# Performance work log

Hardware: AMD Instinct MI355X
Metric: run time of the kernel (lower is better)

The kernel has to match this reference:

```python
import jax, jax.numpy as jnp
import numpy as np

B, N, D_MODEL, H = 2, 2048, 1024, 16
HD = D_MODEL // H  # head_dim = 64

def setup_inputs() -> dict:
    key = jax.random.key(0)
    ks = jax.random.split(key, 5)
    x = jax.random.normal(ks[0], (B, N, D_MODEL), dtype=jnp.float32)
    scale = 0.02
    # Linear weights stored as [in, out] (torch does x @ W.T with W [out,in]; equivalent math)
    Wq = jax.random.normal(ks[1], (D_MODEL, D_MODEL), dtype=jnp.float32) * scale
    Wk = jax.random.normal(ks[2], (D_MODEL, D_MODEL), dtype=jnp.float32) * scale
    Wv = jax.random.normal(ks[3], (D_MODEL, D_MODEL), dtype=jnp.float32) * scale
    Wo = jax.random.normal(ks[4], (D_MODEL, D_MODEL), dtype=jnp.float32) * scale
    return {"x": x, "Wq": Wq, "Wk": Wk, "Wv": Wv, "Wo": Wo}

def reference(x, Wq, Wk, Wv, Wo):
    b, n, _ = x.shape
    # QKV projections (no bias; qkv_bias=False)
    q = (x @ Wq).reshape(b, n, H, HD)
    k = (x @ Wk).reshape(b, n, H, HD)
    v = (x @ Wv).reshape(b, n, H, HD)
    # scores [b, h, q, k]
    scores = jnp.einsum('bqhd,bkhd->bhqk', q, k) / jnp.sqrt(jnp.float32(HD))
    causal = jnp.triu(jnp.ones((n, n), dtype=bool), k=1)  # True above diagonal -> masked
    scores = jnp.where(causal, -jnp.inf, scores)
    attn = jax.nn.softmax(scores, axis=-1)  # dropout p=0.0 -> identity
    ctx = jnp.einsum('bhqk,bkhd->bqhd', attn, v).reshape(b, n, D_MODEL)
    return ctx @ Wo
```

## Files before the change

kernel.cpp:

```cpp
#include <hip/hip_runtime.h>
#include <math.h>

#define D_MODEL 1024
#define NHEAD 16
#define HD 64
#define SEQ 2048
#define BATCH 2
#define MTOT (BATCH * SEQ)

typedef __attribute__((ext_vector_type(8))) short bf16x8;
typedef __attribute__((ext_vector_type(4))) float f32x4;

__device__ __forceinline__ unsigned short f2bf(float f) {
    unsigned int u = __float_as_uint(f);
    u += 0x7FFF + ((u >> 16) & 1);
    return (unsigned short)(u >> 16);
}

__device__ __forceinline__ unsigned int pk2bf(float a, float b) {
    unsigned int r;
    asm("v_cvt_pk_bf16_f32 %0, %1, %2" : "=v"(r) : "v"(a), "v"(b));
    return r;
}

__device__ __forceinline__ void async16(unsigned short* lds, const unsigned short* g) {
    __builtin_amdgcn_global_load_lds(
        (const __attribute__((address_space(1))) unsigned int*)g,
        (__attribute__((address_space(3))) unsigned int*)lds, 16, 0, 0);
}

__global__ __launch_bounds__(256) void prep(const float* __restrict__ x,
                                            unsigned short* __restrict__ xb,
                                            const float* __restrict__ W0,
                                            const float* __restrict__ W1,
                                            const float* __restrict__ W2,
                                            const float* __restrict__ W3,
                                            unsigned short* __restrict__ Wt) {
    const int bid = blockIdx.x;
    const int tid = threadIdx.x;
    if (bid < 4096) {
        const int i = (bid * 256 + tid) * 4;
        float4 v = *(const float4*)(x + i);
        uint2 pk;
        pk.x = pk2bf(v.x, v.y);
        pk.y = pk2bf(v.z, v.w);
        *(uint2*)(xb + i) = pk;
    } else {
        __shared__ float T[32][33];
        const int t = bid - 4096;
        const int z = t >> 10, rem = t & 1023;
        const int n0 = (rem & 31) * 32, k0 = (rem >> 5) * 32;
        const float* W = (z == 0) ? W0 : (z == 1) ? W1 : (z == 2) ? W2 : W3;
        unsigned short* out = Wt + (size_t)z * D_MODEL * D_MODEL;
        const int tx = tid & 31, ty = tid >> 5;
#pragma unroll
        for (int i = 0; i < 4; ++i)
            T[ty + 8 * i][tx] = W[(size_t)(k0 + ty + 8 * i) * D_MODEL + n0 + tx];
        __syncthreads();
#pragma unroll
        for (int i = 0; i < 4; ++i)
            out[(size_t)(n0 + ty + 8 * i) * D_MODEL + k0 + tx] = f2bf(T[tx][ty + 8 * i]);
    }
}

template <int MODE>
__global__ __launch_bounds__(256) void gemm_mfma(const unsigned short* __restrict__ A,
                                                 const unsigned short* __restrict__ Wt,
                                                 unsigned short* __restrict__ q,
                                                 unsigned short* __restrict__ k,
                                                 unsigned short* __restrict__ vt,
                                                 float* __restrict__ outf) {
    __shared__ unsigned short SM[16384];
    const int tid = threadIdx.x;
    const int z = blockIdx.z;
    const unsigned short* B = Wt + (size_t)z * D_MODEL * D_MODEL;
    const int m0 = blockIdx.y * 128, n0 = blockIdx.x * 128;
    const int wave = tid >> 6, lane = tid & 63;
    const int quad = lane >> 4, l16 = lane & 15;
    const int wm = wave & 1, wn = wave >> 1;

    f32x4 acc[4][4];
#pragma unroll
    for (int mt = 0; mt < 4; ++mt)
#pragma unroll
        for (int nt = 0; nt < 4; ++nt)
            acc[mt][nt] = (f32x4){0.f, 0.f, 0.f, 0.f};

    for (int k0 = 0; k0 < D_MODEL; k0 += 64) {
        __syncthreads();
#pragma unroll
        for (int i = 0; i < 4; ++i) {
            const int c = i * 256 + tid;
            const int r = c >> 3, cc = (c & 7) * 8;
            const int cbase = i * 256 + wave * 64;
            async16(SM + cbase * 8, A + (size_t)(m0 + r) * D_MODEL + k0 + cc);
            async16(SM + 8192 + cbase * 8, B + (size_t)(n0 + r) * D_MODEL + k0 + cc);
        }
        __syncthreads();
#pragma unroll
        for (int ks = 0; ks < 2; ++ks) {
            bf16x8 af[4], bfr[4];
#pragma unroll
            for (int mt = 0; mt < 4; ++mt)
                af[mt] = *(const bf16x8*)&SM[(wm * 64 + mt * 16 + l16) * 64 + ks * 32 + quad * 8];
#pragma unroll
            for (int nt = 0; nt < 4; ++nt)
                bfr[nt] = *(const bf16x8*)&SM[8192 + (wn * 64 + nt * 16 + l16) * 64 + ks * 32 + quad * 8];
#pragma unroll
            for (int mt = 0; mt < 4; ++mt)
#pragma unroll
                for (int nt = 0; nt < 4; ++nt)
                    acc[mt][nt] = __builtin_amdgcn_mfma_f32_16x16x32_bf16(
                        af[mt], bfr[nt], acc[mt][nt], 0, 0, 0);
        }
    }

    if (MODE == 1) {
#pragma unroll
        for (int mt = 0; mt < 4; ++mt)
#pragma unroll
            for (int nt = 0; nt < 4; ++nt)
#pragma unroll
                for (int reg = 0; reg < 4; ++reg) {
                    const int m = m0 + wm * 64 + mt * 16 + quad * 4 + reg;
                    const int n = n0 + wn * 64 + nt * 16 + l16;
                    outf[(size_t)m * D_MODEL + n] = acc[mt][nt][reg];
                }
    } else if (z < 2) {
        const float qsc = (z == 0) ? 0.18033688011112042f : 1.0f;
        unsigned short* dst = (z == 0) ? q : k;
        const int bb = m0 >> 11;
        const int tok0 = m0 & (SEQ - 1);
        const int h0 = n0 >> 6;
#pragma unroll
        for (int pass = 0; pass < 2; ++pass) {
            __syncthreads();
            if (wm == pass) {
#pragma unroll
                for (int mt = 0; mt < 4; ++mt)
#pragma unroll
                    for (int nt = 0; nt < 4; ++nt)
#pragma unroll
                        for (int reg = 0; reg < 4; ++reg) {
                            const int r = mt * 16 + quad * 4 + reg;
                            const int cc = wn * 64 + nt * 16 + l16;
                            SM[r * 128 + cc] = f2bf(acc[mt][nt][reg] * qsc);
                        }
            }
            __syncthreads();
#pragma unroll
            for (int it = 0; it < 4; ++it) {
                const int cix = it * 256 + tid;
                const int r = cix >> 4, g = cix & 15;
                const int hh = g >> 3, d8 = g & 7;
                uint4 val = *(const uint4*)&SM[r * 128 + g * 8];
                *(uint4*)(dst + (((size_t)bb * NHEAD + h0 + hh) * SEQ +
                                 tok0 + pass * 64 + r) * HD + d8 * 8) = val;
            }
        }
    } else {
        const int bb = m0 >> 11, tok0 = m0 & (SEQ - 1);
#pragma unroll
        for (int pass = 0; pass < 2; ++pass) {
            __syncthreads();
            if (wn == pass) {
#pragma unroll
                for (int mt = 0; mt < 4; ++mt)
#pragma unroll
                    for (int nt = 0; nt < 4; ++nt) {
                        const int d = nt * 16 + l16;
                        const int m = wm * 64 + mt * 16 + quad * 4;
                        uint2 w;
                        w.x = pk2bf(acc[mt][nt][0], acc[mt][nt][1]);
                        w.y = pk2bf(acc[mt][nt][2], acc[mt][nt][3]);
                        *(uint2*)&SM[d * 136 + m] = w;
                    }
            }
            __syncthreads();
            const int h = (n0 >> 6) + pass;
#pragma unroll
            for (int it = 0; it < 4; ++it) {
                const int c = it * 256 + tid;
                const int d = c >> 4, mc = (c & 15) * 8;
                uint4 val = *(const uint4*)&SM[d * 136 + mc];
                *(uint4*)(vt + (((size_t)bb * NHEAD + h) * HD + d) * SEQ + tok0 + mc) = val;
            }
        }
    }
}

__global__ __launch_bounds__(256, 2) void attn_mfma(const unsigned short* __restrict__ Q,
                                                    const unsigned short* __restrict__ K,
                                                    const unsigned short* __restrict__ VT,
                                                    unsigned short* __restrict__ ctx) {
    __shared__ float CMB[8832];
    const int tid = threadIdx.x;
    const int wave = tid >> 6, lane = tid & 63;
    const int quad = lane >> 4, l16 = lane & 15;
    const int h = blockIdx.x, b = blockIdx.z;
    const int y = blockIdx.y;
    const unsigned short* Qp = Q + ((size_t)b * NHEAD + h) * SEQ * HD;
    const unsigned short* Kp = K + ((size_t)b * NHEAD + h) * SEQ * HD;
    const unsigned short* Vp = VT + ((size_t)b * NHEAD + h) * HD * SEQ;
    unsigned short* Pw = (unsigned short*)CMB + wave * 4096;
    const int sw8 = l16 & 7;

#pragma unroll 1
    for (int half = 0; half < 2; ++half) {
        const int p = half ? y : (31 - y);
        const int row0 = p * 64;
        if (half) __syncthreads();

        bf16x8 bQ[4][2];
#pragma unroll
        for (int f = 0; f < 4; ++f)
#pragma unroll
            for (int ks = 0; ks < 2; ++ks)
                bQ[f][ks] = *(const bf16x8*)(Qp +
                    (size_t)(row0 + f * 16 + l16) * HD + ks * 32 + quad * 8);

        f32x4 o[4][4];
        float ps[4] = {0.f, 0.f, 0.f, 0.f};
#pragma unroll
        for (int nt = 0; nt < 4; ++nt)
#pragma unroll
            for (int f = 0; f < 4; ++f)
                o[nt][f] = (f32x4){0.f, 0.f, 0.f, 0.f};

        for (int kt = wave; kt <= p; kt += 4) {
            bf16x8 aK[4][2], aV[4][2];
#pragma unroll
            for (int mt = 0; mt < 4; ++mt)
#pragma unroll
                for (int ks = 0; ks < 2; ++ks)
                    aK[mt][ks] = *(const bf16x8*)(Kp +
                        (size_t)(kt * 64 + mt * 16 + l16) * HD + ks * 32 + quad * 8);
#pragma unroll
            for (int nt = 0; nt < 4; ++nt)
#pragma unroll
                for (int ks = 0; ks < 2; ++ks)
                    aV[nt][ks] = *(const bf16x8*)(Vp +
                        (size_t)(nt * 16 + l16) * SEQ + kt * 64 + ks * 32 + quad * 8);

            f32x4 sT[4][4];
            __builtin_amdgcn_s_setprio(1);
#pragma unroll
            for (int mt = 0; mt < 4; ++mt)
#pragma unroll
                for (int f = 0; f < 4; ++f) {
                    sT[mt][f] = __builtin_amdgcn_mfma_f32_16x16x32_bf16(
                        aK[mt][0], bQ[f][0], (f32x4){0.f, 0.f, 0.f, 0.f}, 0, 0, 0);
                    sT[mt][f] = __builtin_amdgcn_mfma_f32_16x16x32_bf16(
                        aK[mt][1], bQ[f][1], sT[mt][f], 0, 0, 0);
                }
            __builtin_amdgcn_s_setprio(0);

            const bool diag = (kt == p);
#pragma unroll
            for (int mt = 0; mt < 4; ++mt)
#pragma unroll
                for (int f = 0; f < 4; ++f) {
                    float pv[4];
#pragma unroll
                    for (int reg = 0; reg < 4; ++reg)
                        pv[reg] = exp2f(sT[mt][f][reg]);
                    if (diag) {
                        const int kb = kt * 64 + mt * 16 + quad * 4;
                        const int qg = row0 + f * 16 + l16;
#pragma unroll
                        for (int reg = 0; reg < 4; ++reg)
                            pv[reg] = (kb + reg > qg) ? 0.f : pv[reg];
                    }
                    ps[f] += (pv[0] + pv[1]) + (pv[2] + pv[3]);
                    uint2 w;
                    w.x = pk2bf(pv[0], pv[1]);
                    w.y = pk2bf(pv[2], pv[3]);
                    const int gph = ((mt * 2 + (quad >> 1)) ^ sw8);
                    *(uint2*)&Pw[(f * 16 + l16) * 64 + gph * 8 + (quad & 1) * 4] = w;
                }

            bf16x8 bP[4][2];
#pragma unroll
            for (int f = 0; f < 4; ++f)
#pragma unroll
                for (int ks = 0; ks < 2; ++ks)
                    bP[f][ks] = *(const bf16x8*)&Pw[(f * 16 + l16) * 64 +
                                                    ((ks * 4 + quad) ^ sw8) * 8];

            __builtin_amdgcn_s_setprio(1);
#pragma unroll
            for (int nt = 0; nt < 4; ++nt)
#pragma unroll
                for (int f = 0; f < 4; ++f) {
                    o[nt][f] = __builtin_amdgcn_mfma_f32_16x16x32_bf16(
                        aV[nt][0], bP[f][0], o[nt][f], 0, 0, 0);
                    o[nt][f] = __builtin_amdgcn_mfma_f32_16x16x32_bf16(
                        aV[nt][1], bP[f][1], o[nt][f], 0, 0, 0);
                }
            __builtin_amdgcn_s_setprio(0);
        }

#pragma unroll
        for (int f = 0; f < 4; ++f) {
            ps[f] += __shfl_xor(ps[f], 16);
            ps[f] += __shfl_xor(ps[f], 32);
        }

        __syncthreads();
        if (wave >= 2) {
            float* Rg = CMB + (wave - 2) * 4352;
#pragma unroll
            for (int nt = 0; nt < 4; ++nt)
#pragma unroll
                for (int f = 0; f < 4; ++f)
                    *(f32x4*)&Rg[(f * 16 + l16) * 68 + nt * 16 + quad * 4] = o[nt][f];
            if (quad == 0)
#pragma unroll
                for (int f = 0; f < 4; ++f)
                    CMB[8704 + (wave - 2) * 64 + f * 16 + l16] = ps[f];
        }
        __syncthreads();
        if (wave < 2) {
            float* Rg = CMB + wave * 4352;
#pragma unroll
            for (int nt = 0; nt < 4; ++nt)
#pragma unroll
                for (int f = 0; f < 4; ++f)
                    o[nt][f] += *(const f32x4*)&Rg[(f * 16 + l16) * 68 + nt * 16 + quad * 4];
#pragma unroll
            for (int f = 0; f < 4; ++f)
                ps[f] += CMB[8704 + wave * 64 + f * 16 + l16];
        }
        __syncthreads();
        if (wave == 1) {
#pragma unroll
            for (int nt = 0; nt < 4; ++nt)
#pragma unroll
                for (int f = 0; f < 4; ++f)
                    *(f32x4*)&CMB[(f * 16 + l16) * 68 + nt * 16 + quad * 4] = o[nt][f];
            if (quad == 0)
#pragma unroll
                for (int f = 0; f < 4; ++f)
                    CMB[8704 + f * 16 + l16] = ps[f];
        }
        __syncthreads();
        if (wave == 0) {
#pragma unroll
            for (int nt = 0; nt < 4; ++nt)
#pragma unroll
                for (int f = 0; f < 4; ++f)
                    o[nt][f] += *(const f32x4*)&CMB[(f * 16 + l16) * 68 + nt * 16 + quad * 4];
            float inv[4];
#pragma unroll
            for (int f = 0; f < 4; ++f)
                inv[f] = 1.f / (ps[f] + CMB[8704 + f * 16 + l16]);
#pragma unroll
            for (int nt = 0; nt < 4; ++nt)
#pragma unroll
                for (int f = 0; f < 4; ++f) {
                    const int tok = row0 + f * 16 + l16;
                    const int col = h * HD + nt * 16 + quad * 4;
                    uint2 w;
                    w.x = pk2bf(o[nt][f][0] * inv[f], o[nt][f][1] * inv[f]);
                    w.y = pk2bf(o[nt][f][2] * inv[f], o[nt][f][3] * inv[f]);
                    *(uint2*)(ctx + ((size_t)b * SEQ + tok) * D_MODEL + col) = w;
                }
        }
    }
}

extern "C" void kernel_launch(void* const* d_in, const int* in_sizes, int n_in,
                              void* d_out, int out_size, void* d_ws, size_t ws_size,
                              hipStream_t stream) {
    const float* x  = (const float*)d_in[0];
    const float* Wq = (const float*)d_in[1];
    const float* Wk = (const float*)d_in[2];
    const float* Wv = (const float*)d_in[3];
    const float* Wo = (const float*)d_in[4];
    float* out = (float*)d_out;

    unsigned short* ws = (unsigned short*)d_ws;
    const size_t T = (size_t)MTOT * D_MODEL;
    unsigned short* xb  = ws;
    unsigned short* Wt  = ws + T;
    unsigned short* q   = ws + 2 * T;
    unsigned short* k   = ws + 3 * T;
    unsigned short* vt  = ws + 4 * T;
    unsigned short* ctx = ws + 5 * T;

    prep<<<dim3(8192), dim3(256), 0, stream>>>(x, xb, Wq, Wk, Wv, Wo, Wt);

    gemm_mfma<0><<<dim3(8, 32, 3), dim3(256), 0, stream>>>(xb, Wt, q, k, vt, nullptr);

    attn_mfma<<<dim3(NHEAD, 16, BATCH), dim3(256), 0, stream>>>(q, k, vt, ctx);

    gemm_mfma<1><<<dim3(8, 32, 1), dim3(256), 0, stream>>>(ctx, Wt + 3 * (size_t)D_MODEL * D_MODEL,
                                                           nullptr, nullptr, nullptr, out);
}
```

Baseline: 206.3 us.

## Rewrite QKV projection GEMM with 256x256 tiles, double-buffered async loads and swizzled LDS

Replaces the templated QKV GEMM with a dedicated 512-thread kernel that computes 256x256 output tiles. K-slices are double-buffered in 128KB of LDS and the next tile's global-to-LDS loads are interleaved with MFMA compute using split barriers and vmcnt waits. The LDS layout uses an XOR swizzle to avoid bank conflicts, and a block-index swizzle improves L2 reuse. The output projection keeps the old 128x128 kernel, renamed. The trade-off is heavy register and LDS use and only 192 blocks, which may underfill the GPU's compute units.

Result: faster. 189.0 us (-8.4%).

```diff
diff --git a/kernel.cpp b/kernel.cpp
--- a/kernel.cpp
+++ b/kernel.cpp
@@ -27,6 +27,12 @@
     __builtin_amdgcn_global_load_lds(
         (const __attribute__((address_space(1))) unsigned int*)g,
         (__attribute__((address_space(3))) unsigned int*)lds, 16, 0, 0);
+}
+
+__device__ __forceinline__ void BAR() {
+    asm volatile("" ::: "memory");
+    __builtin_amdgcn_s_barrier();
+    asm volatile("" ::: "memory");
 }
 
 __global__ __launch_bounds__(256) void prep(const float* __restrict__ x,
@@ -63,17 +69,185 @@
     }
 }
 
-template <int MODE>
-__global__ __launch_bounds__(256) void gemm_mfma(const unsigned short* __restrict__ A,
-                                                 const unsigned short* __restrict__ Wt,
-                                                 unsigned short* __restrict__ q,
-                                                 unsigned short* __restrict__ k,
-                                                 unsigned short* __restrict__ vt,
-                                                 float* __restrict__ outf) {
+__global__ __launch_bounds__(512, 2) void qkv_mfma(const unsigned short* __restrict__ A,
+                                                   const unsigned short* __restrict__ Wt,
+                                                   unsigned short* __restrict__ q,
+                                                   unsigned short* __restrict__ k,
+                                                   unsigned short* __restrict__ vt) {
+    __shared__ unsigned short SM[65536];
+    const int tid = threadIdx.x;
+    const int wave = tid >> 6, lane = tid & 63;
+    const int quad = lane >> 4, l16 = lane & 15;
+    const int wm = wave >> 2, wn = wave & 3;
+
+    const int bid = blockIdx.x;
+    const int swz = (bid & 7) * 24 + (bid >> 3);
+    const int by = swz / 12, bx = swz % 12;
+    const int m0 = by * 256;
+    const int z = bx >> 2, c0 = (bx & 3) * 256;
+    const unsigned short* Bz = Wt + (size_t)z * D_MODEL * D_MODEL;
+
+    const unsigned short* aptr[2];
+    const unsigned short* bptr[2];
+    int ldsoff[2];
+#pragma unroll
+    for (int j = 0; j < 2; ++j) {
+        const int s = j * 512 + tid;
+        const int r = s >> 2;
+        const int cg = (s & 3) ^ ((r + (r >> 2)) & 3);
+        aptr[j] = A + (size_t)(m0 + r) * D_MODEL + cg * 8;
+        bptr[j] = Bz + (size_t)(c0 + r) * D_MODEL + cg * 8;
+        ldsoff[j] = (j * 512 + wave * 64) * 8;
+    }
+
+    const int key = (l16 + (l16 >> 2)) & 3;
+    const int chunk = quad ^ key;
+    int aoff[8], boff[4];
+#pragma unroll
+    for (int mt = 0; mt < 8; ++mt)
+        aoff[mt] = ((wm * 128 + mt * 16 + l16) * 4 + chunk) * 8;
+#pragma unroll
+    for (int nt = 0; nt < 4; ++nt)
+        boff[nt] = 16384 + ((wn * 64 + nt * 16 + l16) * 4 + chunk) * 8;
+
+    f32x4 acc[8][4];
+#pragma unroll
+    for (int mt = 0; mt < 8; ++mt)
+#pragma unroll
+        for (int nt = 0; nt < 4; ++nt)
+            acc[mt][nt] = (f32x4){0.f, 0.f, 0.f, 0.f};
+
+    auto stage = [&](int d, int op, int ks, int T) {
+        const int base = d * 32768 + op * 16384 + ks * 8192;
+#pragma unroll
+        for (int j = 0; j < 2; ++j)
+            async16(SM + base + ldsoff[j],
+                    (op ? bptr[j] : aptr[j]) + T * 64 + ks * 32);
+    };
+    auto dsA = [&](bf16x8* af, int mh, int d, int ks) {
+        const int base = d * 32768 + ks * 8192;
+#pragma unroll
+        for (int i = 0; i < 4; ++i)
+            af[i] = *(const bf16x8*)&SM[base + aoff[mh * 4 + i]];
+    };
+    auto dsB = [&](bf16x8* bf, int d, int ks) {
+        const int base = d * 32768 + ks * 8192;
+#pragma unroll
+        for (int i = 0; i < 4; ++i)
+            bf[i] = *(const bf16x8*)&SM[base + boff[i]];
+    };
+    auto mfma16 = [&](bf16x8* af, bf16x8* bf, int mh) {
+        __builtin_amdgcn_s_setprio(1);
+#pragma unroll
+        for (int i = 0; i < 4; ++i)
+#pragma unroll
+            for (int nt = 0; nt < 4; ++nt)
+                acc[mh * 4 + i][nt] = __builtin_amdgcn_mfma_f32_16x16x32_bf16(
+                    af[i], bf[nt], acc[mh * 4 + i][nt], 0, 0, 0);
+        __builtin_amdgcn_s_setprio(0);
+    };
+
+    stage(0, 0, 0, 0);
+    stage(0, 1, 0, 0);
+    stage(0, 0, 1, 0);
+    stage(0, 1, 1, 0);
+    asm volatile("s_waitcnt vmcnt(4)" ::: "memory");
+    BAR();
+
+    const int NT = D_MODEL / 64;
+    for (int T = 0; T < NT; ++T) {
+        const int d = T & 1, dn = d ^ 1;
+        const bool nx = (T + 1 < NT);
+        bf16x8 af[4], bf[4];
+        if (nx) stage(dn, 0, 0, T + 1);
+        dsA(af, 0, d, 0);
+        dsB(bf, d, 0);
+        mfma16(af, bf, 0);
+        BAR();
+        if (nx) stage(dn, 1, 0, T + 1);
+        dsA(af, 1, d, 0);
+        mfma16(af, bf, 1);
+        if (nx) asm volatile("s_waitcnt vmcnt(4)" ::: "memory");
+        else    asm volatile("s_waitcnt vmcnt(0)" ::: "memory");
+        BAR();
+        if (nx) stage(dn, 0, 1, T + 1);
+        dsA(af, 0, d, 1);
+        dsB(bf, d, 1);
+        mfma16(af, bf, 0);
+        BAR();
+        if (nx) stage(dn, 1, 1, T + 1);
+        dsA(af, 1, d, 1);
+        mfma16(af, bf, 1);
+        if (nx) asm volatile("s_waitcnt vmcnt(4)" ::: "memory");
+        else    asm volatile("s_waitcnt vmcnt(0)" ::: "memory");
+        BAR();
+    }
+
+    __syncthreads();
+    const int bb = m0 >> 11, tok0 = m0 & (SEQ - 1), h0 = c0 >> 6;
+    if (z < 2) {
+        const float qsc = (z == 0) ? 0.18033688011112042f : 1.0f;
+        unsigned short* dst = (z == 0) ? q : k;
+#pragma unroll
+        for (int pass = 0; pass < 2; ++pass) {
+            if (pass) __syncthreads();
+            if (wm == pass) {
+#pragma unroll
+                for (int mt = 0; mt < 8; ++mt)
+#pragma unroll
+                    for (int nt = 0; nt < 4; ++nt)
+#pragma unroll
+                        for (int reg = 0; reg < 4; ++reg) {
+                            const int rr = mt * 16 + quad * 4 + reg;
+                            const int cc = wn * 64 + nt * 16 + l16;
+                            SM[rr * 264 + cc] = f2bf(acc[mt][nt][reg] * qsc);
+                        }
+            }
+            __syncthreads();
+#pragma unroll
+            for (int it = 0; it < 8; ++it) {
+                const int g = it * 512 + tid;
+                const int r = g >> 5, gg = g & 31;
+                uint4 val = *(const uint4*)&SM[r * 264 + gg * 8];
+                *(uint4*)(dst + (((size_t)bb * NHEAD + h0 + (gg >> 3)) * SEQ +
+                                 tok0 + pass * 128 + r) * HD + (gg & 7) * 8) = val;
+            }
+        }
+    } else {
+#pragma unroll
+        for (int pass = 0; pass < 2; ++pass) {
+            if (pass) __syncthreads();
+            if (wm == pass) {
+#pragma unroll
+                for (int mt = 0; mt < 8; ++mt)
+#pragma unroll
+                    for (int nt = 0; nt < 4; ++nt) {
+                        const int dd = wn * 64 + nt * 16 + l16;
+                        const int m = mt * 16 + quad * 4;
+                        uint2 w;
+                        w.x = pk2bf(acc[mt][nt][0], acc[mt][nt][1]);
+                        w.y = pk2bf(acc[mt][nt][2], acc[mt][nt][3]);
+                        *(uint2*)&SM[dd * 136 + m] = w;
+                    }
+            }
+            __syncthreads();
+#pragma unroll
+            for (int it = 0; it < 8; ++it) {
+                const int g = it * 512 + tid;
+                const int dd = g >> 4, tg = (g & 15) * 8;
+                uint4 val = *(const uint4*)&SM[dd * 136 + tg];
+                *(uint4*)(vt + (((size_t)bb * NHEAD + h0 + (dd >> 6)) * HD + (dd & 63)) * SEQ +
+                          tok0 + pass * 128 + tg) = val;
+            }
+        }
+    }
+}
+
+__global__ __launch_bounds__(256) void gemm_out(const unsigned short* __restrict__ A,
+                                                const unsigned short* __restrict__ Bw,
+                                                float* __restrict__ outf) {
     __shared__ unsigned short SM[16384];
     const int tid = threadIdx.x;
-    const int z = blockIdx.z;
-    const unsigned short* B = Wt + (size_t)z * D_MODEL * D_MODEL;
     const int m0 = blockIdx.y * 128, n0 = blockIdx.x * 128;
     const int wave = tid >> 6, lane = tid & 63;
     const int quad = lane >> 4, l16 = lane & 15;
@@ -94,7 +268,7 @@
             const int r = c >> 3, cc = (c & 7) * 8;
             const int cbase = i * 256 + wave * 64;
             async16(SM + cbase * 8, A + (size_t)(m0 + r) * D_MODEL + k0 + cc);
-            async16(SM + 8192 + cbase * 8, B + (size_t)(n0 + r) * D_MODEL + k0 + cc);
+            async16(SM + 8192 + cbase * 8, Bw + (size_t)(n0 + r) * D_MODEL + k0 + cc);
         }
         __syncthreads();
 #pragma unroll
@@ -115,78 +289,16 @@
         }
     }
 
-    if (MODE == 1) {
-#pragma unroll
-        for (int mt = 0; mt < 4; ++mt)
-#pragma unroll
-            for (int nt = 0; nt < 4; ++nt)
-#pragma unroll
-                for (int reg = 0; reg < 4; ++reg) {
-                    const int m = m0 + wm * 64 + mt * 16 + quad * 4 + reg;
-                    const int n = n0 + wn * 64 + nt * 16 + l16;
-                    outf[(size_t)m * D_MODEL + n] = acc[mt][nt][reg];
-                }
-    } else if (z < 2) {
-        const float qsc = (z == 0) ? 0.18033688011112042f : 1.0f;
-        unsigned short* dst = (z == 0) ? q : k;
-        const int bb = m0 >> 11;
-        const int tok0 = m0 & (SEQ - 1);
-        const int h0 = n0 >> 6;
-#pragma unroll
-        for (int pass = 0; pass < 2; ++pass) {
-            __syncthreads();
-            if (wm == pass) {
-#pragma unroll
-                for (int mt = 0; mt < 4; ++mt)
-#pragma unroll
-                    for (int nt = 0; nt < 4; ++nt)
-#pragma unroll
-                        for (int reg = 0; reg < 4; ++reg) {
-                            const int r = mt * 16 + quad * 4 + reg;
-                            const int cc = wn * 64 + nt * 16 + l16;
-                            SM[r * 128 + cc] = f2bf(acc[mt][nt][reg] * qsc);
-                        }
+#pragma unroll
+    for (int mt = 0; mt < 4; ++mt)
+#pragma unroll
+        for (int nt = 0; nt < 4; ++nt)
+#pragma unroll
+            for (int reg = 0; reg < 4; ++reg) {
+                const int m = m0 + wm * 64 + mt * 16 + quad * 4 + reg;
+                const int n = n0 + wn * 64 + nt * 16 + l16;
+                outf[(size_t)m * D_MODEL + n] = acc[mt][nt][reg];
             }
-            __syncthreads();
-#pragma unroll
-            for (int it = 0; it < 4; ++it) {
-                const int cix = it * 256 + tid;
-                const int r = cix >> 4, g = cix & 15;
-                const int hh = g >> 3, d8 = g & 7;
-                uint4 val = *(const uint4*)&SM[r * 128 + g * 8];
-                *(uint4*)(dst + (((size_t)bb * NHEAD + h0 + hh) * SEQ +
-                                 tok0 + pass * 64 + r) * HD + d8 * 8) = val;
-            }
-        }
-    } else {
-        const int bb = m0 >> 11, tok0 = m0 & (SEQ - 1);
-#pragma unroll
-        for (int pass = 0; pass < 2; ++pass) {
-            __syncthreads();
-            if (wn == pass) {
-#pragma unroll
-                for (int mt = 0; mt < 4; ++mt)
-#pragma unroll
-                    for (int nt = 0; nt < 4; ++nt) {
-                        const int d = nt * 16 + l16;
-                        const int m = wm * 64 + mt * 16 + quad * 4;
-                        uint2 w;
-                        w.x = pk2bf(acc[mt][nt][0], acc[mt][nt][1]);
-                        w.y = pk2bf(acc[mt][nt][2], acc[mt][nt][3]);
-                        *(uint2*)&SM[d * 136 + m] = w;
-                    }
-            }
-            __syncthreads();
-            const int h = (n0 >> 6) + pass;
-#pragma unroll
-            for (int it = 0; it < 4; ++it) {
-                const int c = it * 256 + tid;
-                const int d = c >> 4, mc = (c & 15) * 8;
-                uint4 val = *(const uint4*)&SM[d * 136 + mc];
-                *(uint4*)(vt + (((size_t)bb * NHEAD + h) * HD + d) * SEQ + tok0 + mc) = val;
-            }
-        }
-    }
 }
 
 __global__ __launch_bounds__(256, 2) void attn_mfma(const unsigned short* __restrict__ Q,
@@ -390,10 +502,9 @@
 
     prep<<<dim3(8192), dim3(256), 0, stream>>>(x, xb, Wq, Wk, Wv, Wo, Wt);
 
-    gemm_mfma<0><<<dim3(8, 32, 3), dim3(256), 0, stream>>>(xb, Wt, q, k, vt, nullptr);
+    qkv_mfma<<<dim3(192), dim3(512), 0, stream>>>(xb, Wt, q, k, vt);
 
     attn_mfma<<<dim3(NHEAD, 16, BATCH), dim3(256), 0, stream>>>(q, k, vt, ctx);
 
-    gemm_mfma<1><<<dim3(8, 32, 1), dim3(256), 0, stream>>>(ctx, Wt + 3 * (size_t)D_MODEL * D_MODEL,
-                                                           nullptr, nullptr, nullptr, out);
-}
+    gemm_out<<<dim3(8, 32), dim3(256), 0, stream>>>(ctx, Wt + 3 * (size_t)D_MODEL * D_MODEL, out);
+}
```
